# Kernel tuning notes

Measured on AMD Instinct MI355X. Metric: run time of the kernel, lower is better.

Reference implementation:

```python
import jax, jax.numpy as jnp
import numpy as np

MODEL_DIM = 1024
NUM_HEADS = 16
DEPTH = MODEL_DIM // NUM_HEADS


def setup_inputs() -> dict:
    key = jax.random.key(0)
    ks = jax.random.split(key, 9)
    B, S, D = 4, 2048, MODEL_DIM
    scale = 1.0 / np.sqrt(D)
    x = jax.random.normal(ks[0], (B, S, D), dtype=jnp.float32)
    wq = jax.random.normal(ks[1], (D, D), dtype=jnp.float32) * scale
    bq = jnp.zeros((D,), dtype=jnp.float32)
    wk = jax.random.normal(ks[2], (D, D), dtype=jnp.float32) * scale
    bk = jnp.zeros((D,), dtype=jnp.float32)
    wv = jax.random.normal(ks[3], (D, D), dtype=jnp.float32) * scale
    bv = jnp.zeros((D,), dtype=jnp.float32)
    wo = jax.random.normal(ks[4], (D, D), dtype=jnp.float32) * scale
    bo = jnp.zeros((D,), dtype=jnp.float32)
    return {"x": x, "wq": wq, "bq": bq, "wk": wk, "bk": bk,
            "wv": wv, "bv": bv, "wo": wo, "bo": bo}


def reference(x, wq, bq, wk, bk, wv, bv, wo, bo):
    B, S, D = x.shape
    H, dh = NUM_HEADS, DEPTH
    # projections
    q = (x @ wq + bq).reshape(B, S, H, dh).transpose(0, 2, 1, 3)  # [B,H,S,dh]
    k = (x @ wk + bk).reshape(B, S, H, dh).transpose(0, 2, 1, 3)
    v = (x @ wv + bv).reshape(B, S, H, dh).transpose(0, 2, 1, 3)
    # scaled dot-product attention (full score matrix, as in source)
    logits = jnp.einsum('bhqd,bhkd->bhqk', q, k) / jnp.sqrt(jnp.float32(dh))
    attn = jax.nn.softmax(logits, axis=-1)
    out = jnp.einsum('bhqk,bhkd->bhqd', attn, v)  # [B,H,S,dh]
    out = out.transpose(0, 2, 1, 3).reshape(B, S, D)
    return out @ wo + bo
```

## Files before the change

kernel.cpp:

```cpp
#include <hip/hip_runtime.h>
#include <hip/hip_bf16.h>


#define S_LEN 2048
#define DMODEL 1024
#define NH 16
#define DH 64
#define BATCH 4
#define MROWS (BATCH * S_LEN)
#define NELEM_X (MROWS * DMODEL)
#define NELEM_W (DMODEL * DMODEL)
#define NELEM_B DMODEL

typedef short short8 __attribute__((ext_vector_type(8)));
typedef float floatx4 __attribute__((ext_vector_type(4)));

__device__ __forceinline__ float bf2f(unsigned short u) {
    union { unsigned int i; float f; } c; c.i = ((unsigned int)u) << 16; return c.f;
}
__device__ __forceinline__ unsigned int f2bf_pk(float lo, float hi) {
    unsigned int r;
    asm("v_cvt_pk_bf16_f32 %0, %1, %2" : "=v"(r) : "v"(lo), "v"(hi));
    return r;
}
__device__ __forceinline__ void async_copy16(const void* g, void* l) {
    __builtin_amdgcn_global_load_lds(
        (const __attribute__((address_space(1))) unsigned int*)g,
        (__attribute__((address_space(3))) unsigned int*)l, 16, 0, 0);
}

__global__ void sniff_kernel(const unsigned short* __restrict__ x, int* flag) {
    __shared__ int cnt;
    if (threadIdx.x == 0) cnt = 0;
    __syncthreads();
    int c = 0;
    for (int i = threadIdx.x; i < 65536; i += 256) {
        unsigned int e = (x[i] >> 7) & 0xFFu;
        if (e >= 0xC0u) c++;
    }
    atomicAdd(&cnt, c);
    __syncthreads();
    if (threadIdx.x == 0) *flag = (cnt > 64) ? 1 : 0;
}

struct ConvArgs { const void* s[5]; unsigned short* d[5]; int n8[5]; };
__global__ void convert_all(ConvArgs a, const int* __restrict__ flag) {
    const int seg = blockIdx.y;
    const int f = *flag;
    const int n8 = a.n8[seg];
    unsigned short* dst = a.d[seg];
    int i = blockIdx.x * blockDim.x + threadIdx.x;
    const int stride = gridDim.x * blockDim.x;
    if (f) {
        const float4* s4 = (const float4*)a.s[seg];
        for (; i < n8; i += stride) {
            float4 x0 = s4[2 * i], x1 = s4[2 * i + 1];
            uint4 o;
            o.x = f2bf_pk(x0.x, x0.y); o.y = f2bf_pk(x0.z, x0.w);
            o.z = f2bf_pk(x1.x, x1.y); o.w = f2bf_pk(x1.z, x1.w);
            *(uint4*)(dst + (size_t)i * 8) = o;
        }
    } else {
        const uint4* s4 = (const uint4*)a.s[seg];
        for (; i < n8; i += stride) *(uint4*)(dst + (size_t)i * 8) = s4[i];
    }
}

struct TWArgs { const void* s[4]; unsigned short* d[4]; };
__global__ void transpose_w(TWArgs a, const int* __restrict__ flag) {
    __shared__ unsigned int Lt[64 * 33];
    const int z = blockIdx.z;
    const int f = *flag;
    const int k0 = blockIdx.x * 64, n0 = blockIdx.y * 64;
    const int t = threadIdx.x;
    const int c = t & 63, rgrp = t >> 6;

    if (f) {
        const float* W = (const float*)a.s[z];
        #pragma unroll
        for (int s = 0; s < 8; s++) {
            int r0 = rgrp * 16 + 2 * s;
            float v0 = W[(size_t)(k0 + r0) * DMODEL + n0 + c];
            float v1 = W[(size_t)(k0 + r0 + 1) * DMODEL + n0 + c];
            Lt[c * 33 + rgrp * 8 + s] = f2bf_pk(v0, v1);
        }
    } else {
        const unsigned short* W = (const unsigned short*)a.s[z];
        #pragma unroll
        for (int s = 0; s < 8; s++) {
            int r0 = rgrp * 16 + 2 * s;
            unsigned int lo = W[(size_t)(k0 + r0) * DMODEL + n0 + c];
            unsigned int hi = W[(size_t)(k0 + r0 + 1) * DMODEL + n0 + c];
            Lt[c * 33 + rgrp * 8 + s] = lo | (hi << 16);
        }
    }
    __syncthreads();
    const int row = t >> 2, j = t & 3;
    unsigned int* outp = (unsigned int*)(a.d[z] + (size_t)(n0 + row) * DMODEL + k0);
    #pragma unroll
    for (int i = 0; i < 8; i++) outp[j * 8 + i] = Lt[row * 33 + j * 8 + i];
}

__global__ void transpose_v(const unsigned short* __restrict__ vws,
                            unsigned short* __restrict__ vt) {
    __shared__ unsigned int Lt[64 * 33];
    const int tok0 = blockIdx.x * 64;
    const int bh   = blockIdx.y;
    const int b    = bh >> 4;
    const int h    = bh & 15;
    const int t = threadIdx.x;
    const int c = t & 63, rgrp = t >> 6;

    const unsigned short* src = vws + (size_t)b * S_LEN * DMODEL + h * DH;
    #pragma unroll
    for (int s = 0; s < 8; s++) {
        int r0 = rgrp * 16 + 2 * s;
        unsigned int lo = src[(size_t)(tok0 + r0) * DMODEL + c];
        unsigned int hi = src[(size_t)(tok0 + r0 + 1) * DMODEL + c];
        Lt[c * 33 + rgrp * 8 + s] = lo | (hi << 16);
    }
    __syncthreads();
    const int row = t >> 2, j = t & 3;
    unsigned int* outp = (unsigned int*)(vt + (size_t)bh * DH * S_LEN
                                            + (size_t)row * S_LEN + tok0);
    #pragma unroll
    for (int i = 0; i < 8; i++) outp[j * 8 + i] = Lt[row * 33 + j * 8 + i];
}

__global__ __launch_bounds__(256, 2)
void gemm_bias_kernel(const unsigned short* __restrict__ X,
                      const unsigned short* __restrict__ T0, const unsigned short* __restrict__ B0, void* __restrict__ Y0,
                      const unsigned short* __restrict__ T1, const unsigned short* __restrict__ B1, void* __restrict__ Y1,
                      const unsigned short* __restrict__ T2, const unsigned short* __restrict__ B2, void* __restrict__ Y2,
                      float os0, float os1, float os2,
                      const int* __restrict__ flag, int fp32_out)
{
    const unsigned short* Wt = T0; const unsigned short* Bi = B0; void* Y = Y0;
    float os = os0;
    if (blockIdx.z == 1) { Wt = T1; Bi = B1; Y = Y1; os = os1; }
    else if (blockIdx.z == 2) { Wt = T2; Bi = B2; Y = Y2; os = os2; }
    const int f32o = fp32_out ? (*flag) : 0;

    __shared__ __align__(16) unsigned short As[128 * 32];
    __shared__ __align__(16) unsigned short Bs[128 * 32];

    const int t    = threadIdx.x;
    const int lane = t & 63;
    const int wid  = t >> 6;
    const int quad = lane >> 4;
    const int n16  = lane & 15;
    const int wm   = wid >> 1, wn = wid & 1;

    const int m0 = blockIdx.x * 128;
    const int n0 = blockIdx.y * 128;

    floatx4 acc[4][4];
    #pragma unroll
    for (int i = 0; i < 4; i++)
        #pragma unroll
        for (int j = 0; j < 4; j++) acc[i][j] = (floatx4){0.f, 0.f, 0.f, 0.f};

    const int r = t >> 2, c8 = (t & 3) * 8;

    for (int kb = 0; kb < DMODEL; kb += 32) {
        __syncthreads();
        async_copy16(X  + (size_t)(m0 + r)      * DMODEL + kb + c8, As + r * 32 + c8);
        async_copy16(X  + (size_t)(m0 + 64 + r) * DMODEL + kb + c8, As + (64 + r) * 32 + c8);
        async_copy16(Wt + (size_t)(n0 + r)      * DMODEL + kb + c8, Bs + r * 32 + c8);
        async_copy16(Wt + (size_t)(n0 + 64 + r) * DMODEL + kb + c8, Bs + (64 + r) * 32 + c8);
        __syncthreads();

        short8 af[4], bfr[4];
        #pragma unroll
        for (int mt = 0; mt < 4; mt++)
            af[mt] = *(const short8*)(As + (wm * 64 + mt * 16 + n16) * 32 + quad * 8);
        #pragma unroll
        for (int nt = 0; nt < 4; nt++)
            bfr[nt] = *(const short8*)(Bs + (wn * 64 + nt * 16 + n16) * 32 + quad * 8);
        #pragma unroll
        for (int mt = 0; mt < 4; mt++)
            #pragma unroll
            for (int nt = 0; nt < 4; nt++)
                acc[mt][nt] = __builtin_amdgcn_mfma_f32_16x16x32_bf16(af[mt], bfr[nt], acc[mt][nt], 0, 0, 0);
    }

    float bv4[4];
    #pragma unroll
    for (int nt = 0; nt < 4; nt++) bv4[nt] = bf2f(Bi[n0 + wn * 64 + nt * 16 + n16]) * os;
    #pragma unroll
    for (int mt = 0; mt < 4; mt++)
        #pragma unroll
        for (int rr = 0; rr < 4; rr++) {
            size_t row = (size_t)(m0 + wm * 64 + mt * 16 + quad * 4 + rr);
            if (f32o) {
                #pragma unroll
                for (int nt = 0; nt < 4; nt++) {
                    int col = n0 + wn * 64 + nt * 16 + n16;
                    ((float*)Y)[row * DMODEL + col] = fmaf(acc[mt][nt][rr], os, bv4[nt]);
                }
            } else {
                #pragma unroll
                for (int np = 0; np < 2; np++) {
                    float v0 = fmaf(acc[mt][2 * np    ][rr], os, bv4[2 * np]);
                    float v1 = fmaf(acc[mt][2 * np + 1][rr], os, bv4[2 * np + 1]);
                    unsigned int pk = f2bf_pk(v0, v1);
                    int col = n0 + wn * 64 + (2 * np) * 16 + n16;
                    ((unsigned short*)Y)[row * DMODEL + col]      = (unsigned short)pk;
                    ((unsigned short*)Y)[row * DMODEL + col + 16] = (unsigned short)(pk >> 16);
                }
            }
        }
}

__global__ __launch_bounds__(256, 4)
void attn_kernel(const unsigned short* Qw,
                 const unsigned short* __restrict__ Kw,
                 const unsigned short* __restrict__ VT,
                 unsigned short* Ow)
{
    __shared__ __align__(16) unsigned short Ks[64 * 72];
    __shared__ __align__(16) unsigned short Vts[64 * 72];
    __shared__ __align__(16) unsigned short Ps[4 * 16 * 72];

    const int t    = threadIdx.x;
    const int lane = t & 63;
    const int w    = t >> 6;
    const int quad = lane >> 4;
    const int n16  = lane & 15;

    const int bid  = blockIdx.x;
    const int bh   = bid & 63;
    const int qblk = bid >> 6;
    const int b    = bh >> 4;
    const int h    = bh & 15;

    const size_t baseRow = (size_t)b * S_LEN;
    const int hoff = h * DH;
    const unsigned short* VTb = VT + (size_t)bh * DH * S_LEN;

    int qrow[2];
    short8 qf[2][2];
    #pragma unroll
    for (int g = 0; g < 2; g++) {
        qrow[g] = qblk * 128 + w * 32 + g * 16 + n16;
        qf[g][0] = *(const short8*)(Qw + (baseRow + qrow[g]) * DMODEL + hoff + quad * 8);
        qf[g][1] = *(const short8*)(Qw + (baseRow + qrow[g]) * DMODEL + hoff + 32 + quad * 8);
    }

    floatx4 acco[2][4];
    #pragma unroll
    for (int g = 0; g < 2; g++)
        #pragma unroll
        for (int i = 0; i < 4; i++) acco[g][i] = (floatx4){0.f, 0.f, 0.f, 0.f};
    float ls[2] = {0.f, 0.f};

    const int krow = t >> 3, kchk = (t & 7) * 8;
    const int vrow = t >> 2, vchk = (t & 3) * 16;

    const unsigned short* Kp0 = Kw + (baseRow + krow)      * DMODEL + hoff + kchk;
    const unsigned short* Kp1 = Kw + (baseRow + krow + 32) * DMODEL + hoff + kchk;
    const unsigned short* Vp  = VTb + (size_t)vrow * S_LEN + vchk;

    float4 kr0 = *(const float4*)(Kp0);
    float4 kr1 = *(const float4*)(Kp1);
    float4 vr0 = *(const float4*)(Vp);
    float4 vr1 = *(const float4*)(Vp + 8);

    for (int kb = 0; kb < S_LEN; kb += 64) {
        __syncthreads();
        *(float4*)(Ks + krow * 72 + kchk)        = kr0;
        *(float4*)(Ks + (krow + 32) * 72 + kchk) = kr1;
        *(float4*)(Vts + vrow * 72 + vchk)       = vr0;
        *(float4*)(Vts + vrow * 72 + vchk + 8)   = vr1;
        if (kb + 64 < S_LEN) {
            kr0 = *(const float4*)(Kp0 + (size_t)(kb + 64) * DMODEL);
            kr1 = *(const float4*)(Kp1 + (size_t)(kb + 64) * DMODEL);
            vr0 = *(const float4*)(Vp + kb + 64);
            vr1 = *(const float4*)(Vp + kb + 72);
        }
        __syncthreads();

        floatx4 sf[2][4];
        #pragma unroll
        for (int g = 0; g < 2; g++)
            #pragma unroll
            for (int kt = 0; kt < 4; kt++) sf[g][kt] = (floatx4){0.f, 0.f, 0.f, 0.f};
        #pragma unroll
        for (int kt = 0; kt < 4; kt++)
            #pragma unroll
            for (int ks = 0; ks < 2; ks++) {
                short8 kf = *(const short8*)(Ks + (kt * 16 + n16) * 72 + ks * 32 + quad * 8);
                #pragma unroll
                for (int g = 0; g < 2; g++)
                    sf[g][kt] = __builtin_amdgcn_mfma_f32_16x16x32_bf16(kf, qf[g][ks], sf[g][kt], 0, 0, 0);
            }

        unsigned short* Pw = Ps + w * 16 * 72;
        unsigned int*   Pu = (unsigned int*)Pw;
        short8 pf[2][2];
        #pragma unroll
        for (int g = 0; g < 2; g++) {
            float lsum = 0.f;
            #pragma unroll
            for (int kt = 0; kt < 4; kt++)
                #pragma unroll
                for (int rr = 0; rr < 4; rr++) {
                    float p = __builtin_exp2f(sf[g][kt][rr]);
                    sf[g][kt][rr] = p;
                    lsum += p;
                }
            ls[g] += lsum;
            #pragma unroll
            for (int kt = 0; kt < 4; kt++) {
                uint2 pk2 = make_uint2(f2bf_pk(sf[g][kt][0], sf[g][kt][1]),
                                       f2bf_pk(sf[g][kt][2], sf[g][kt][3]));
                *(uint2*)(Pu + n16 * 36 + kt * 8 + quad * 2) = pk2;
            }
            __asm__ volatile("" ::: "memory");
            pf[g][0] = *(const short8*)(Pw + n16 * 72 + quad * 8);
            pf[g][1] = *(const short8*)(Pw + n16 * 72 + 32 + quad * 8);
            __asm__ volatile("" ::: "memory");
        }

        #pragma unroll
        for (int ks = 0; ks < 2; ks++)
            #pragma unroll
            for (int dt = 0; dt < 4; dt++) {
                short8 vf = *(const short8*)(Vts + (dt * 16 + n16) * 72 + ks * 32 + quad * 8);
                #pragma unroll
                for (int g = 0; g < 2; g++)
                    acco[g][dt] = __builtin_amdgcn_mfma_f32_16x16x32_bf16(vf, pf[g][ks], acco[g][dt], 0, 0, 0);
            }
    }

    #pragma unroll
    for (int g = 0; g < 2; g++) {
        float l = ls[g];
        l += __shfl_xor(l, 16);
        l += __shfl_xor(l, 32);
        const float rinv = 1.f / l;
        #pragma unroll
        for (int dt = 0; dt < 4; dt++) {
            uint2 o;
            o.x = f2bf_pk(acco[g][dt][0] * rinv, acco[g][dt][1] * rinv);
            o.y = f2bf_pk(acco[g][dt][2] * rinv, acco[g][dt][3] * rinv);
            *(uint2*)(Ow + (baseRow + qrow[g]) * DMODEL + hoff + dt * 16 + quad * 4) = o;
        }
    }
}

extern "C" void kernel_launch(void* const* d_in, const int* in_sizes, int n_in,
                              void* d_out, int out_size, void* d_ws, size_t ws_size,
                              hipStream_t stream)
{
    unsigned short* base = (unsigned short*)d_ws;
    int* flag = (int*)d_ws;
    unsigned short* xc  = base + 8;
    unsigned short* wqt = xc  + NELEM_X;
    unsigned short* wkt = wqt + NELEM_W;
    unsigned short* wvt = wkt + NELEM_W;
    unsigned short* wot = wvt + NELEM_W;
    unsigned short* bqc = wot + NELEM_W;
    unsigned short* bkc = bqc + NELEM_B;
    unsigned short* bvc = bkc + NELEM_B;
    unsigned short* boc = bvc + NELEM_B;
    unsigned short* qws = boc + NELEM_B;
    unsigned short* kws = qws + NELEM_X;
    unsigned short* vws = kws + NELEM_X;
    unsigned short* aws = qws;
    unsigned short* vtw = xc;

    sniff_kernel<<<1, 256, 0, stream>>>((const unsigned short*)d_in[0], flag);

    ConvArgs ca;
    const void* csrc[5] = {d_in[0], d_in[2], d_in[4], d_in[6], d_in[8]};
    unsigned short* cdst[5] = {xc, bqc, bkc, bvc, boc};
    int cn8[5] = {NELEM_X / 8, NELEM_B / 8, NELEM_B / 8, NELEM_B / 8, NELEM_B / 8};
    for (int i = 0; i < 5; i++) { ca.s[i] = csrc[i]; ca.d[i] = cdst[i]; ca.n8[i] = cn8[i]; }
    convert_all<<<dim3(256, 5), 256, 0, stream>>>(ca, flag);

    TWArgs tw;
    const void* tsrc[4] = {d_in[1], d_in[3], d_in[5], d_in[7]};
    unsigned short* tdst[4] = {wqt, wkt, wvt, wot};
    for (int i = 0; i < 4; i++) { tw.s[i] = tsrc[i]; tw.d[i] = tdst[i]; }
    transpose_w<<<dim3(16, 16, 4), 256, 0, stream>>>(tw, flag);

    const float qscale = 0.125f * 1.44269504088896340736f;
    gemm_bias_kernel<<<dim3(64, 8, 3), 256, 0, stream>>>(
        xc, wqt, bqc, qws, wkt, bkc, kws, wvt, bvc, vws,
        qscale, 1.f, 1.f, flag, 0);

    transpose_v<<<dim3(32, 64), 256, 0, stream>>>(vws, vtw);

    attn_kernel<<<dim3(1024), 256, 0, stream>>>(qws, kws, vtw, aws);

    gemm_bias_kernel<<<dim3(64, 8, 1), 256, 0, stream>>>(
        aws, wot, boc, d_out, wot, boc, d_out, wot, boc, d_out,
        1.f, 1.f, 1.f, flag, 1);
}
```

Baseline: 426.1 us.

## Rewrite attention kernel with 32x32x16 MFMA and register-resident P

Switches the attention kernel from 16x16x32 to 32x32x16 bf16 MFMA tiles, doubling query rows per block (256) and halving the grid. P is fed directly from registers into the PV MFMA, with V columns permuted in transpose_v to match the accumulator layout, which removes the LDS round-trip for P. K/V shared tiles use an XOR swizzle instead of padding, and s_setprio is raised around MFMA sections. Occupancy drops to 2 blocks per CU and register pressure rises, and only 512 blocks are launched.

```diff
diff --git a/kernel.cpp b/kernel.cpp
--- a/kernel.cpp
+++ b/kernel.cpp
@@ -14,6 +14,7 @@
 
 typedef short short8 __attribute__((ext_vector_type(8)));
 typedef float floatx4 __attribute__((ext_vector_type(4)));
+typedef float floatx16 __attribute__((ext_vector_type(16)));
 
 __device__ __forceinline__ float bf2f(unsigned short u) {
     union { unsigned int i; float f; } c; c.i = ((unsigned int)u) << 16; return c.f;
@@ -27,6 +28,10 @@
     __builtin_amdgcn_global_load_lds(
         (const __attribute__((address_space(1))) unsigned int*)g,
         (__attribute__((address_space(3))) unsigned int*)l, 16, 0, 0);
+}
+
+__device__ __forceinline__ floatx16 mfma32_k16(short8 a, short8 b, floatx16 c) {
+    return __builtin_amdgcn_mfma_f32_32x32x16_bf16(a, b, c, 0, 0, 0);
 }
 
 __global__ void sniff_kernel(const unsigned short* __restrict__ x, int* flag) {
@@ -123,8 +128,9 @@
     const int row = t >> 2, j = t & 3;
     unsigned int* outp = (unsigned int*)(vt + (size_t)bh * DH * S_LEN
                                             + (size_t)row * S_LEN + tok0);
-    #pragma unroll
-    for (int i = 0; i < 8; i++) outp[j * 8 + i] = Lt[row * 33 + j * 8 + i];
+    const int p2[8] = {0, 1, 4, 5, 2, 3, 6, 7};
+    #pragma unroll
+    for (int i = 0; i < 8; i++) outp[j * 8 + i] = Lt[row * 33 + j * 8 + p2[i]];
 }
 
 __global__ __launch_bounds__(256, 2)
@@ -212,21 +218,21 @@
         }
 }
 
-__global__ __launch_bounds__(256, 4)
+__global__ __launch_bounds__(256, 2)
 void attn_kernel(const unsigned short* Qw,
                  const unsigned short* __restrict__ Kw,
                  const unsigned short* __restrict__ VT,
                  unsigned short* Ow)
 {
-    __shared__ __align__(16) unsigned short Ks[64 * 72];
-    __shared__ __align__(16) unsigned short Vts[64 * 72];
-    __shared__ __align__(16) unsigned short Ps[4 * 16 * 72];
+    __shared__ __align__(16) unsigned short Ks[64 * 64];
+    __shared__ __align__(16) unsigned short Vts[64 * 64];
 
     const int t    = threadIdx.x;
     const int lane = t & 63;
     const int w    = t >> 6;
-    const int quad = lane >> 4;
-    const int n16  = lane & 15;
+    const int q32  = lane & 31;
+    const int hi   = lane >> 5;
+    const int r7   = q32 & 7;
 
     const int bid  = blockIdx.x;
     const int bh   = bid & 63;
@@ -239,112 +245,126 @@
     const unsigned short* VTb = VT + (size_t)bh * DH * S_LEN;
 
     int qrow[2];
-    short8 qf[2][2];
+    short8 qf[2][4];
     #pragma unroll
     for (int g = 0; g < 2; g++) {
-        qrow[g] = qblk * 128 + w * 32 + g * 16 + n16;
-        qf[g][0] = *(const short8*)(Qw + (baseRow + qrow[g]) * DMODEL + hoff + quad * 8);
-        qf[g][1] = *(const short8*)(Qw + (baseRow + qrow[g]) * DMODEL + hoff + 32 + quad * 8);
-    }
-
-    floatx4 acco[2][4];
+        qrow[g] = qblk * 256 + w * 64 + g * 32 + q32;
+        #pragma unroll
+        for (int ds = 0; ds < 4; ds++)
+            qf[g][ds] = *(const short8*)(Qw + (baseRow + qrow[g]) * DMODEL + hoff
+                                            + ds * 16 + hi * 8);
+    }
+
+    const floatx16 z16 = {0.f,0.f,0.f,0.f,0.f,0.f,0.f,0.f,
+                          0.f,0.f,0.f,0.f,0.f,0.f,0.f,0.f};
+    floatx16 acco[2][2];
     #pragma unroll
     for (int g = 0; g < 2; g++)
         #pragma unroll
-        for (int i = 0; i < 4; i++) acco[g][i] = (floatx4){0.f, 0.f, 0.f, 0.f};
+        for (int dt = 0; dt < 2; dt++) acco[g][dt] = z16;
     float ls[2] = {0.f, 0.f};
 
-    const int krow = t >> 3, kchk = (t & 7) * 8;
-    const int vrow = t >> 2, vchk = (t & 3) * 16;
-
-    const unsigned short* Kp0 = Kw + (baseRow + krow)      * DMODEL + hoff + kchk;
-    const unsigned short* Kp1 = Kw + (baseRow + krow + 32) * DMODEL + hoff + kchk;
-    const unsigned short* Vp  = VTb + (size_t)vrow * S_LEN + vchk;
-
-    float4 kr0 = *(const float4*)(Kp0);
-    float4 kr1 = *(const float4*)(Kp1);
-    float4 vr0 = *(const float4*)(Vp);
-    float4 vr1 = *(const float4*)(Vp + 8);
+    const int srow = t >> 2;
+    const int scc  = (t & 3) * 2;
+    const int kswz0 = ((scc    ) ^ (srow & 7)) * 8;
+    const int kswz1 = ((scc + 1) ^ (srow & 7)) * 8;
+    unsigned short* KsW = Ks  + srow * 64;
+    unsigned short* VsW = Vts + srow * 64;
+    const unsigned short* Kp = Kw + (baseRow + srow) * DMODEL + hoff;
+    const unsigned short* Vp = VTb + (size_t)srow * S_LEN;
+
+    float4 kr0 = *(const float4*)(Kp + scc * 8);
+    float4 kr1 = *(const float4*)(Kp + scc * 8 + 8);
+    float4 vr0 = *(const float4*)(Vp + scc * 8);
+    float4 vr1 = *(const float4*)(Vp + scc * 8 + 8);
 
     for (int kb = 0; kb < S_LEN; kb += 64) {
         __syncthreads();
-        *(float4*)(Ks + krow * 72 + kchk)        = kr0;
-        *(float4*)(Ks + (krow + 32) * 72 + kchk) = kr1;
-        *(float4*)(Vts + vrow * 72 + vchk)       = vr0;
-        *(float4*)(Vts + vrow * 72 + vchk + 8)   = vr1;
+        *(float4*)(KsW + kswz0) = kr0;
+        *(float4*)(KsW + kswz1) = kr1;
+        *(float4*)(VsW + kswz0) = vr0;
+        *(float4*)(VsW + kswz1) = vr1;
         if (kb + 64 < S_LEN) {
-            kr0 = *(const float4*)(Kp0 + (size_t)(kb + 64) * DMODEL);
-            kr1 = *(const float4*)(Kp1 + (size_t)(kb + 64) * DMODEL);
-            vr0 = *(const float4*)(Vp + kb + 64);
-            vr1 = *(const float4*)(Vp + kb + 72);
+            kr0 = *(const float4*)(Kp + (size_t)(kb + 64) * DMODEL + scc * 8);
+            kr1 = *(const float4*)(Kp + (size_t)(kb + 64) * DMODEL + scc * 8 + 8);
+            vr0 = *(const float4*)(Vp + kb + 64 + scc * 8);
+            vr1 = *(const float4*)(Vp + kb + 64 + scc * 8 + 8);
         }
         __syncthreads();
 
-        floatx4 sf[2][4];
+        floatx16 sf[2][2];
         #pragma unroll
         for (int g = 0; g < 2; g++)
             #pragma unroll
-            for (int kt = 0; kt < 4; kt++) sf[g][kt] = (floatx4){0.f, 0.f, 0.f, 0.f};
-        #pragma unroll
-        for (int kt = 0; kt < 4; kt++)
-            #pragma unroll
-            for (int ks = 0; ks < 2; ks++) {
-                short8 kf = *(const short8*)(Ks + (kt * 16 + n16) * 72 + ks * 32 + quad * 8);
-                #pragma unroll
-                for (int g = 0; g < 2; g++)
-                    sf[g][kt] = __builtin_amdgcn_mfma_f32_16x16x32_bf16(kf, qf[g][ks], sf[g][kt], 0, 0, 0);
+            for (int kt = 0; kt < 2; kt++) sf[g][kt] = z16;
+
+        __builtin_amdgcn_s_setprio(1);
+        #pragma unroll
+        for (int kt = 0; kt < 2; kt++) {
+            const unsigned short* Kr = Ks + (kt * 32 + q32) * 64;
+            #pragma unroll
+            for (int ds = 0; ds < 4; ds++) {
+                short8 kf = *(const short8*)(Kr + (((ds * 2 + hi) ^ r7) * 8));
+                sf[0][kt] = mfma32_k16(kf, qf[0][ds], sf[0][kt]);
+                sf[1][kt] = mfma32_k16(kf, qf[1][ds], sf[1][kt]);
             }
-
-        unsigned short* Pw = Ps + w * 16 * 72;
-        unsigned int*   Pu = (unsigned int*)Pw;
-        short8 pf[2][2];
+        }
+        __builtin_amdgcn_s_setprio(0);
+
         #pragma unroll
         for (int g = 0; g < 2; g++) {
             float lsum = 0.f;
             #pragma unroll
-            for (int kt = 0; kt < 4; kt++)
+            for (int kt = 0; kt < 2; kt++)
                 #pragma unroll
-                for (int rr = 0; rr < 4; rr++) {
-                    float p = __builtin_exp2f(sf[g][kt][rr]);
-                    sf[g][kt][rr] = p;
+                for (int i = 0; i < 16; i++) {
+                    float p = __builtin_exp2f(sf[g][kt][i]);
+                    sf[g][kt][i] = p;
                     lsum += p;
                 }
             ls[g] += lsum;
-            #pragma unroll
-            for (int kt = 0; kt < 4; kt++) {
-                uint2 pk2 = make_uint2(f2bf_pk(sf[g][kt][0], sf[g][kt][1]),
-                                       f2bf_pk(sf[g][kt][2], sf[g][kt][3]));
-                *(uint2*)(Pu + n16 * 36 + kt * 8 + quad * 2) = pk2;
+        }
+
+        __builtin_amdgcn_s_setprio(1);
+        #pragma unroll
+        for (int kt = 0; kt < 2; kt++) {
+            #pragma unroll
+            for (int tt = 0; tt < 2; tt++) {
+                union { unsigned int u[4]; short8 s8; } pb0, pb1;
+                #pragma unroll
+                for (int j = 0; j < 4; j++) {
+                    pb0.u[j] = f2bf_pk(sf[0][kt][8 * tt + 2 * j],
+                                       sf[0][kt][8 * tt + 2 * j + 1]);
+                    pb1.u[j] = f2bf_pk(sf[1][kt][8 * tt + 2 * j],
+                                       sf[1][kt][8 * tt + 2 * j + 1]);
+                }
+                const int vchunk = ((4 * kt + 2 * tt + hi) ^ r7) * 8;
+                #pragma unroll
+                for (int dt = 0; dt < 2; dt++) {
+                    short8 vf = *(const short8*)(Vts + (dt * 32 + q32) * 64 + vchunk);
+                    acco[0][dt] = mfma32_k16(vf, pb0.s8, acco[0][dt]);
+                    acco[1][dt] = mfma32_k16(vf, pb1.s8, acco[1][dt]);
+                }
             }
-            __asm__ volatile("" ::: "memory");
-            pf[g][0] = *(const short8*)(Pw + n16 * 72 + quad * 8);
-            pf[g][1] = *(const short8*)(Pw + n16 * 72 + 32 + quad * 8);
-            __asm__ volatile("" ::: "memory");
-        }
-
-        #pragma unroll
-        for (int ks = 0; ks < 2; ks++)
-            #pragma unroll
-            for (int dt = 0; dt < 4; dt++) {
-                short8 vf = *(const short8*)(Vts + (dt * 16 + n16) * 72 + ks * 32 + quad * 8);
-                #pragma unroll
-                for (int g = 0; g < 2; g++)
-                    acco[g][dt] = __builtin_amdgcn_mfma_f32_16x16x32_bf16(vf, pf[g][ks], acco[g][dt], 0, 0, 0);
-            }
+        }
+        __builtin_amdgcn_s_setprio(0);
     }
 
     #pragma unroll
     for (int g = 0; g < 2; g++) {
         float l = ls[g];
-        l += __shfl_xor(l, 16);
         l += __shfl_xor(l, 32);
         const float rinv = 1.f / l;
         #pragma unroll
-        for (int dt = 0; dt < 4; dt++) {
-            uint2 o;
-            o.x = f2bf_pk(acco[g][dt][0] * rinv, acco[g][dt][1] * rinv);
-            o.y = f2bf_pk(acco[g][dt][2] * rinv, acco[g][dt][3] * rinv);
-            *(uint2*)(Ow + (baseRow + qrow[g]) * DMODEL + hoff + dt * 16 + quad * 4) = o;
+        for (int dt = 0; dt < 2; dt++) {
+            #pragma unroll
+            for (int m = 0; m < 4; m++) {
+                uint2 o;
+                o.x = f2bf_pk(acco[g][dt][4 * m] * rinv, acco[g][dt][4 * m + 1] * rinv);
+                o.y = f2bf_pk(acco[g][dt][4 * m + 2] * rinv, acco[g][dt][4 * m + 3] * rinv);
+                *(uint2*)(Ow + (baseRow + qrow[g]) * DMODEL + hoff
+                             + dt * 32 + m * 8 + hi * 4) = o;
+            }
         }
     }
 }
@@ -392,7 +412,7 @@
 
     transpose_v<<<dim3(32, 64), 256, 0, stream>>>(vws, vtw);
 
-    attn_kernel<<<dim3(1024), 256, 0, stream>>>(qws, kws, vtw, aws);
+    attn_kernel<<<dim3(512), 256, 0, stream>>>(qws, kws, vtw, aws);
 
     gemm_bias_kernel<<<dim3(64, 8, 1), 256, 0, stream>>>(
         aws, wot, boc, d_out, wot, boc, d_out, wot, boc, d_out,
```

Result: faster. 369.5 us (-13.3%).
